# Performance work log

Measured on AMD Instinct MI355X. Metric: run time of the kernel, lower is better.

The kernel has to match this reference:

```python
import jax, jax.numpy as jnp
import numpy as np

V, E, H, B, T, O = 50000, 300, 512, 32, 256, 10


def setup_inputs() -> dict:
    key = jax.random.key(0)
    ks = jax.random.split(key, 12)
    sc = 1.0 / np.sqrt(H)  # torch LSTM init scale
    rn = lambda k, shape, s: (jax.random.normal(k, shape, jnp.float32) * s)
    return {
        "tokens": jax.random.randint(ks[0], (B, T), 0, V),
        "embed_table": rn(ks[1], (V, E), 0.1),
        "W_ih_f": rn(ks[2], (4 * H, E), sc),
        "W_hh_f": rn(ks[3], (4 * H, H), sc),
        "b_ih_f": rn(ks[4], (4 * H,), sc),
        "b_hh_f": rn(ks[5], (4 * H,), sc),
        "W_ih_b": rn(ks[6], (4 * H, E), sc),
        "W_hh_b": rn(ks[7], (4 * H, H), sc),
        "b_ih_b": rn(ks[8], (4 * H,), sc),
        "b_hh_b": rn(ks[9], (4 * H,), sc),
        "W_out": rn(ks[10], (O, 2 * H), 1.0 / np.sqrt(2 * H)),
        "b_out": rn(ks[11], (O,), 0.01),
    }


def _lstm_dir(x_tbe, W_ih, W_hh, b_ih, b_hh, reverse):
    """One LSTM direction. x_tbe: [T,B,E]. Returns hidden seq [T,B,H]."""
    Hd = W_hh.shape[1]
    # precompute input contribution for all timesteps: [T,B,4H]
    xg = jnp.einsum('tbe,ge->tbg', x_tbe, W_ih) + b_ih + b_hh

    def step(carry, xt):
        h, c = carry
        gates = xt + h @ W_hh.T                    # [B,4H]
        i, f, g, o = jnp.split(gates, 4, axis=-1)  # torch gate order i,f,g,o
        c = jax.nn.sigmoid(f) * c + jax.nn.sigmoid(i) * jnp.tanh(g)
        h = jax.nn.sigmoid(o) * jnp.tanh(c)
        return (h, c), h

    h0 = jnp.zeros((x_tbe.shape[1], Hd), x_tbe.dtype)
    _, hs = jax.lax.scan(step, (h0, h0), xg, reverse=reverse)
    return hs


def reference(tokens, embed_table, W_ih_f, W_hh_f, b_ih_f, b_hh_f,
              W_ih_b, W_hh_b, b_ih_b, b_hh_b, W_out, b_out):
    x = embed_table[tokens]          # [B,T,E] embedding lookup (dropout_e=0 in eval)
    x = x.transpose(1, 0, 2)         # [T,B,E] time-major, as in the torch module
    hf = _lstm_dir(x, W_ih_f, W_hh_f, b_ih_f, b_hh_f, reverse=False)
    hb = _lstm_dir(x, W_ih_b, W_hh_b, b_ih_b, b_hh_b, reverse=True)
    rnn_out = jnp.concatenate([hf, hb], axis=-1)   # [T,B,2H]
    # relu then max-pool over the full time axis (kernel = seq_len)
    pooled = jnp.max(jax.nn.relu(rnn_out), axis=0)  # [B,2H]
    logits = pooled @ W_out.T + b_out               # [B,O]
    return logits, rnn_out
```

## Files before the change

### kernel.cpp

```cpp
#include <hip/hip_runtime.h>
#include <hip/hip_bf16.h>

#define B_ 32
#define T_ 256
#define E_ 300
#define EP_ 320
#define H_ 512
#define O_ 10
#define TEAM 32
#define THR 512
#define HPB 16
#define NBLK 512

typedef __attribute__((ext_vector_type(8))) short bf16x8;
typedef __attribute__((ext_vector_type(4))) float f32x4;

__device__ __forceinline__ float bf2f(unsigned short u) {
  unsigned v = ((unsigned)u) << 16; float f; __builtin_memcpy(&f, &v, 4); return f;
}
__device__ __forceinline__ short f2bf(float x) {
  unsigned u; __builtin_memcpy(&u, &x, 4);
  unsigned r = u + 0x7fffu + ((u >> 16) & 1u);
  return (short)(r >> 16);
}

__global__ __launch_bounds__(256) void xprep_k(
    const int* __restrict__ tokens, const float* __restrict__ embed,
    unsigned short* __restrict__ xb)
{
  const int t = blockIdx.x;
  __shared__ int tok_s[B_];
  const int tid = threadIdx.x;
  if (tid < B_) tok_s[tid] = tokens[tid * T_ + t];
  __syncthreads();
  const size_t plane = (size_t)T_ * B_ * EP_;
  unsigned short* hi = xb;
  unsigned short* lo = xb + plane;
  for (int i = tid; i < B_ * E_; i += 256) {
    const int b = i / E_, e = i - b * E_;
    const float v = embed[(size_t)tok_s[b] * E_ + e];
    const short h = f2bf(v);
    const short l = f2bf(v - bf2f((unsigned short)h));
    const size_t o = ((size_t)t * B_ + b) * EP_ + e;
    hi[o] = (unsigned short)h; lo[o] = (unsigned short)l;
  }
  for (int i = tid; i < B_ * (EP_ - E_); i += 256) {
    const int b = i / (EP_ - E_), e = E_ + (i - b * (EP_ - E_));
    const size_t o = ((size_t)t * B_ + b) * EP_ + e;
    hi[o] = 0; lo[o] = 0;
  }
}

__global__ __launch_bounds__(320) void wprep_k(
    const float* __restrict__ Wf, const float* __restrict__ Wb,
    unsigned short* __restrict__ wp)
{
  const int row = blockIdx.x;
  const int dir = blockIdx.y;
  const int e   = threadIdx.x;
  const float* __restrict__ W = dir ? Wb : Wf;
  short h = 0, l = 0;
  if (e < E_) {
    const float v = W[(size_t)row * E_ + e];
    h = f2bf(v);
    l = f2bf(v - bf2f((unsigned short)h));
  }
  const size_t hiB = ((size_t)(dir * 2 + 0)) * 2048 * EP_;
  const size_t loB = ((size_t)(dir * 2 + 1)) * 2048 * EP_;
  wp[hiB + (size_t)row * EP_ + e] = (unsigned short)h;
  wp[loB + (size_t)row * EP_ + e] = (unsigned short)l;
}

__global__ __launch_bounds__(256) void xg_mfma_k(
    const unsigned short* __restrict__ wp,
    const unsigned short* __restrict__ xb,
    const float* __restrict__ bif, const float* __restrict__ bhf,
    const float* __restrict__ bib, const float* __restrict__ bhb,
    __hip_bfloat16* __restrict__ xg)
{
  const int rt  = blockIdx.x;
  const int t   = blockIdx.y;
  const int dir = blockIdx.z;
  const int tid = threadIdx.x;
  const int l = tid & 63, w = tid >> 6;
  const int m = l & 15, q = l >> 4;
  const int rowb = rt * 64 + w * 16;

  const float* __restrict__ bi = dir ? bib : bif;
  const float* __restrict__ bh = dir ? bhb : bhf;

  bf16x8 ahi[10], alo[10];
  {
    const unsigned short* whi =
        wp + ((size_t)(dir * 2 + 0) * 2048 + rowb + m) * EP_ + q * 8;
    const unsigned short* wlo =
        wp + ((size_t)(dir * 2 + 1) * 2048 + rowb + m) * EP_ + q * 8;
    #pragma unroll
    for (int kt = 0; kt < 10; ++kt) {
      ahi[kt] = *(const bf16x8*)(whi + kt * 32);
      alo[kt] = *(const bf16x8*)(wlo + kt * 32);
    }
  }

  const size_t plane = (size_t)T_ * B_ * EP_;
  const unsigned short* xh0 = xb + ((size_t)t * B_ + m     ) * EP_ + q * 8;
  const unsigned short* xh1 = xb + ((size_t)t * B_ + m + 16) * EP_ + q * 8;

  f32x4 acc0 = {0.f, 0.f, 0.f, 0.f}, acc1 = {0.f, 0.f, 0.f, 0.f};
  #pragma unroll
  for (int kt = 0; kt < 10; ++kt) {
    bf16x8 b0h = *(const bf16x8*)(xh0 + kt * 32);
    bf16x8 b0l = *(const bf16x8*)(xh0 + plane + kt * 32);
    bf16x8 b1h = *(const bf16x8*)(xh1 + kt * 32);
    bf16x8 b1l = *(const bf16x8*)(xh1 + plane + kt * 32);
    acc0 = __builtin_amdgcn_mfma_f32_16x16x32_bf16(ahi[kt], b0h, acc0, 0, 0, 0);
    acc0 = __builtin_amdgcn_mfma_f32_16x16x32_bf16(alo[kt], b0h, acc0, 0, 0, 0);
    acc0 = __builtin_amdgcn_mfma_f32_16x16x32_bf16(ahi[kt], b0l, acc0, 0, 0, 0);
    acc1 = __builtin_amdgcn_mfma_f32_16x16x32_bf16(ahi[kt], b1h, acc1, 0, 0, 0);
    acc1 = __builtin_amdgcn_mfma_f32_16x16x32_bf16(alo[kt], b1h, acc1, 0, 0, 0);
    acc1 = __builtin_amdgcn_mfma_f32_16x16x32_bf16(ahi[kt], b1l, acc1, 0, 0, 0);
  }

  const int r4 = rowb + q * 4;
  const float4 bi4 = *(const float4*)(bi + r4);
  const float4 bh4 = *(const float4*)(bh + r4);
  const float bias0 = bi4.x + bh4.x, bias1 = bi4.y + bh4.y;
  const float bias2 = bi4.z + bh4.z, bias3 = bi4.w + bh4.w;
  unsigned short* og =
      (unsigned short*)xg + ((size_t)(dir * T_ + t) * 2048 + r4) * B_;
  og[0 * B_ + m]      = (unsigned short)f2bf(acc0[0] + bias0);
  og[1 * B_ + m]      = (unsigned short)f2bf(acc0[1] + bias1);
  og[2 * B_ + m]      = (unsigned short)f2bf(acc0[2] + bias2);
  og[3 * B_ + m]      = (unsigned short)f2bf(acc0[3] + bias3);
  og[0 * B_ + m + 16] = (unsigned short)f2bf(acc1[0] + bias0);
  og[1 * B_ + m + 16] = (unsigned short)f2bf(acc1[1] + bias1);
  og[2 * B_ + m + 16] = (unsigned short)f2bf(acc1[2] + bias2);
  og[3 * B_ + m + 16] = (unsigned short)f2bf(acc1[3] + bias3);
}

__device__ __forceinline__ float sigm(float x)    { return 1.f / (1.f + __expf(-x)); }
__device__ __forceinline__ float tanhfast(float x){ return 1.f - 2.f / (__expf(2.f * x) + 1.f); }

__global__ __launch_bounds__(THR) void lstm_rec_k(
    const __hip_bfloat16* __restrict__ xg,
    const float* __restrict__ Whf, const float* __restrict__ Whb,
    unsigned short* __restrict__ ht,
    float* __restrict__ pooled,
    unsigned int* __restrict__ slots, unsigned int* __restrict__ elect)
{
  unsigned xcd;
  asm volatile("s_getreg_b32 %0, hwreg(HW_REG_XCC_ID)" : "=s"(xcd));
  xcd &= 7u;

  __shared__ unsigned rank_s;
  if (threadIdx.x == 0)
    rank_s = __hip_atomic_fetch_add(&elect[xcd], 1u, __ATOMIC_RELAXED,
                                    __HIP_MEMORY_SCOPE_AGENT);
  __syncthreads();
  const unsigned rank = rank_s;
  if (xcd > 1u || rank >= TEAM) return;
  const int dir = (int)xcd;

  const float* __restrict__ Wh = dir ? Whb : Whf;
  const int hs  = (int)rank * HPB;
  const int tid = threadIdx.x;
  const int l   = tid & 63;
  const int wid = tid >> 6;
  const int g   = wid & 3;
  const int kh  = wid >> 2;
  const int hh  = tid & 15, bb = tid >> 4;

  extern __shared__ char lds[];
  float* gp = (float*)(lds + 65536);

  bf16x8 ahi[8], alo[8];
  {
    const int m = l & 15, q = l >> 4;
    const float* wrow = Wh + (size_t)(g * H_ + hs + m) * H_ + kh * 256 + q * 8;
    #pragma unroll
    for (int kt = 0; kt < 8; ++kt) {
      const float* wp = wrow + kt * 32;
      #pragma unroll
      for (int j = 0; j < 8; ++j) {
        const float w = wp[j];
        const short hi = f2bf(w);
        ahi[kt][j] = hi;
        alo[kt][j] = f2bf(w - bf2f((unsigned short)hi));
      }
    }
  }

  const unsigned short* __restrict__ xgu = (const unsigned short*)xg;
  const size_t xco = ((size_t)hs + hh) * B_ + bb;

  float c_st = 0.f, pm = 0.f;

  for (int s = 0; s < T_; ++s) {
    const int tt = dir ? (T_ - 1 - s) : s;
    const size_t xb = (size_t)(dir * T_ + tt) * 2048 * B_;
    float x0 = bf2f(__builtin_nontemporal_load(xgu + xb + 0 * H_ * B_ + xco));
    float x1 = bf2f(__builtin_nontemporal_load(xgu + xb + 1 * H_ * B_ + xco));
    float x2 = bf2f(__builtin_nontemporal_load(xgu + xb + 2 * H_ * B_ + xco));
    float x3 = bf2f(__builtin_nontemporal_load(xgu + xb + 3 * H_ * B_ + xco));

    if (s > 0) {
      if (tid < 64) {
        unsigned v = 1u;
        const unsigned int* sp =
            slots + ((size_t)dir * T_ + (s - 1)) * TEAM + (tid & 31);
        int it = 0;
        do {
          if (tid < 32) {
            if (it < 16) {
              asm volatile("global_load_dword %0, %1, off sc0 nt\n\ts_waitcnt vmcnt(0)"
                           : "=v"(v) : "v"(sp) : "memory");
            } else {
              v = __hip_atomic_load(sp, __ATOMIC_RELAXED, __HIP_MEMORY_SCOPE_AGENT);
            }
          }
          ++it;
        } while (__ballot(v == 0u) != 0ull && it < (1 << 22));
      }
      __syncthreads();
      {
        const float4* src = (const float4*)(ht + (size_t)(dir * T_ + (s - 1)) * 32768);
        float4* dst = (float4*)lds;
        #pragma unroll
        for (int i = 0; i < 8; ++i)
          dst[tid + i * THR] = src[tid + i * THR];
      }
      __syncthreads();
      f32x4 acc0 = {0.f, 0.f, 0.f, 0.f}, acc1 = {0.f, 0.f, 0.f, 0.f};
      {
        const int n0 = l & 15;
        const int swz = (n0 & 7) << 4;
        const int kb = kh * 512 + (l >> 4) * 16;
        #pragma unroll
        for (int kt = 0; kt < 8; ++kt) {
          const int ko = kb + kt * 64;
          const char* p0 = lds + (((n0      ) * 1024 + ko) ^ swz);
          const char* p1 = lds + (((n0 + 16 ) * 1024 + ko) ^ swz);
          bf16x8 b0h = *(const bf16x8*)(p0);
          bf16x8 b0l = *(const bf16x8*)(p0 + 32768);
          bf16x8 b1h = *(const bf16x8*)(p1);
          bf16x8 b1l = *(const bf16x8*)(p1 + 32768);
          acc0 = __builtin_amdgcn_mfma_f32_16x16x32_bf16(ahi[kt], b0h, acc0, 0, 0, 0);
          acc0 = __builtin_amdgcn_mfma_f32_16x16x32_bf16(alo[kt], b0h, acc0, 0, 0, 0);
          acc0 = __builtin_amdgcn_mfma_f32_16x16x32_bf16(ahi[kt], b0l, acc0, 0, 0, 0);
          acc1 = __builtin_amdgcn_mfma_f32_16x16x32_bf16(ahi[kt], b1h, acc1, 0, 0, 0);
          acc1 = __builtin_amdgcn_mfma_f32_16x16x32_bf16(alo[kt], b1h, acc1, 0, 0, 0);
          acc1 = __builtin_amdgcn_mfma_f32_16x16x32_bf16(ahi[kt], b1l, acc1, 0, 0, 0);
        }
      }
      {
        const int slot = (kh * 4 + g) * 32;
        const int rowb = (l >> 4) * 4;
        #pragma unroll
        for (int r = 0; r < 4; ++r) {
          gp[(slot + (l & 15)     ) * 17 + rowb + r] = acc0[r];
          gp[(slot + 16 + (l & 15)) * 17 + rowb + r] = acc1[r];
        }
      }
      __syncthreads();
    }

    float Gi = x0, Gf = x1, Gg = x2, Go = x3;
    if (s > 0) {
      Gi += gp[(0 * 32 + bb) * 17 + hh] + gp[(4 * 32 + bb) * 17 + hh];
      Gf += gp[(1 * 32 + bb) * 17 + hh] + gp[(5 * 32 + bb) * 17 + hh];
      Gg += gp[(2 * 32 + bb) * 17 + hh] + gp[(6 * 32 + bb) * 17 + hh];
      Go += gp[(3 * 32 + bb) * 17 + hh] + gp[(7 * 32 + bb) * 17 + hh];
    }
    c_st = sigm(Gf) * c_st + sigm(Gi) * tanhfast(Gg);
    const float h = sigm(Go) * tanhfast(c_st);
    pm = fmaxf(pm, h);
    {
      const short hi = f2bf(h);
      const short lo = f2bf(h - bf2f((unsigned short)hi));
      char* base = (char*)(ht + (size_t)(dir * T_ + s) * 32768);
      const unsigned off = (unsigned)((bb * 1024 + (hs + hh) * 2) ^ ((bb & 7) << 4));
      *(unsigned short*)(base + off)         = (unsigned short)hi;
      *(unsigned short*)(base + 32768 + off) = (unsigned short)lo;
    }
    asm volatile("s_waitcnt vmcnt(0)" ::: "memory");
    __syncthreads();
    if (tid == 0) {
      unsigned int* mp = slots + ((size_t)dir * T_ + s) * TEAM + rank;
      unsigned one = 1u;
      asm volatile("global_store_dword %0, %1, off\n\ts_waitcnt vmcnt(0)"
                   :: "v"(mp), "v"(one) : "memory");
    }
  }
  pooled[(size_t)bb * 1024 + dir * H_ + hs + hh] = pm;
}

__global__ __launch_bounds__(256) void finalize_k(
    const unsigned short* __restrict__ ht, float* __restrict__ rnn)
{
  const int t = blockIdx.x, dir = blockIdx.y;
  const int s = dir ? (T_ - 1 - t) : t;
  const char* base = (const char*)(ht + (size_t)(dir * T_ + s) * 32768);
  const int b = threadIdx.x >> 3, c = threadIdx.x & 7;
  float* __restrict__ dst = rnn + ((size_t)t * B_ + b) * 1024 + dir * H_;
  #pragma unroll
  for (int j = 0; j < 8; ++j) {
    const int k0 = (c * 8 + j) * 8;
    const unsigned off = (unsigned)((b * 1024 + k0 * 2) ^ ((b & 7) << 4));
    bf16x8 hi = *(const bf16x8*)(base + off);
    bf16x8 lo = *(const bf16x8*)(base + 32768 + off);
    float4 o0, o1;
    o0.x = bf2f((unsigned short)hi[0]) + bf2f((unsigned short)lo[0]);
    o0.y = bf2f((unsigned short)hi[1]) + bf2f((unsigned short)lo[1]);
    o0.z = bf2f((unsigned short)hi[2]) + bf2f((unsigned short)lo[2]);
    o0.w = bf2f((unsigned short)hi[3]) + bf2f((unsigned short)lo[3]);
    o1.x = bf2f((unsigned short)hi[4]) + bf2f((unsigned short)lo[4]);
    o1.y = bf2f((unsigned short)hi[5]) + bf2f((unsigned short)lo[5]);
    o1.z = bf2f((unsigned short)hi[6]) + bf2f((unsigned short)lo[6]);
    o1.w = bf2f((unsigned short)hi[7]) + bf2f((unsigned short)lo[7]);
    *(float4*)(dst + k0)     = o0;
    *(float4*)(dst + k0 + 4) = o1;
  }
}

__global__ __launch_bounds__(64) void logits_k(
    const float* __restrict__ pooled, const float* __restrict__ Wout,
    const float* __restrict__ bout, float* __restrict__ out)
{
  const int b = blockIdx.x, lane = threadIdx.x;
  float acc[O_];
  #pragma unroll
  for (int o = 0; o < O_; ++o) acc[o] = 0.f;
  for (int k = lane; k < 2 * H_; k += 64) {
    const float pv = pooled[(size_t)b * 1024 + k];
    #pragma unroll
    for (int o = 0; o < O_; ++o) acc[o] += pv * Wout[(size_t)o * 1024 + k];
  }
  #pragma unroll
  for (int o = 0; o < O_; ++o) {
    float v = acc[o];
    #pragma unroll
    for (int off = 32; off > 0; off >>= 1) v += __shfl_down(v, off);
    if (lane == 0) out[b * O_ + o] = v + bout[o];
  }
}

extern "C" void kernel_launch(void* const* d_in, const int* in_sizes, int n_in,
                              void* d_out, int out_size, void* d_ws, size_t ws_size,
                              hipStream_t stream)
{
  const int*   tokens = (const int*)d_in[0];
  const float* embed  = (const float*)d_in[1];
  const float* Wihf   = (const float*)d_in[2];
  const float* Whhf   = (const float*)d_in[3];
  const float* bihf   = (const float*)d_in[4];
  const float* bhhf   = (const float*)d_in[5];
  const float* Wihb   = (const float*)d_in[6];
  const float* Whhb   = (const float*)d_in[7];
  const float* bihb   = (const float*)d_in[8];
  const float* bhhb   = (const float*)d_in[9];
  const float* Wout   = (const float*)d_in[10];
  const float* bout   = (const float*)d_in[11];
  float* out = (float*)d_out;

  char* ws = (char*)d_ws;
  const size_t XG_BYTES = (size_t)2 * T_ * 2048 * B_ * 2;
  const size_t HT_BYTES = (size_t)2 * T_ * 2 * B_ * H_ * 2;
  const size_t PL_BYTES = (size_t)B_ * 1024 * 4;
  const size_t SL_BYTES = (size_t)2 * T_ * TEAM * 4;
  const size_t EL_BYTES = 8 * 4;
  if (ws_size < XG_BYTES + HT_BYTES + PL_BYTES + SL_BYTES + EL_BYTES) return;

  __hip_bfloat16* xg     = (__hip_bfloat16*)ws;
  unsigned short* ht     = (unsigned short*)(ws + XG_BYTES);
  float*          pooled = (float*)(ws + XG_BYTES + HT_BYTES);
  unsigned int*   slots  = (unsigned int*)(ws + XG_BYTES + HT_BYTES + PL_BYTES);
  unsigned int*   elect  = (unsigned int*)(ws + XG_BYTES + HT_BYTES + PL_BYTES + SL_BYTES);

  unsigned short* xb = (unsigned short*)(ws + XG_BYTES);
  unsigned short* wpre = (unsigned short*)(ws + XG_BYTES + (size_t)2 * T_ * B_ * EP_ * 2);

  (void)hipMemsetAsync(slots, 0, SL_BYTES + EL_BYTES, stream);

  xprep_k<<<dim3(T_), 256, 0, stream>>>(tokens, embed, xb);
  wprep_k<<<dim3(2048, 2), 320, 0, stream>>>(Wihf, Wihb, wpre);
  xg_mfma_k<<<dim3(32, T_, 2), 256, 0, stream>>>(wpre, xb, bihf, bhhf, bihb, bhhb, xg);

  const int rec_lds = 82944;
  (void)hipFuncSetAttribute((const void*)lstm_rec_k,
                            hipFuncAttributeMaxDynamicSharedMemorySize, rec_lds);
  lstm_rec_k<<<dim3(NBLK), THR, rec_lds, stream>>>(xg, Whhf, Whhb, ht, pooled,
                                                   slots, elect);

  finalize_k<<<dim3(T_, 2), 256, 0, stream>>>(ht, out + B_ * O_);
  logits_k<<<dim3(B_), 64, 0, stream>>>(pooled, Wout, bout, out);
}
```

Before: 3.322 ms.

## Store per-block hidden-state slabs contiguously and swizzle during LDS load

```diff
diff --git a/kernel.cpp b/kernel.cpp
--- a/kernel.cpp
+++ b/kernel.cpp
@@ -224,10 +224,20 @@
       __syncthreads();
       {
         const float4* src = (const float4*)(ht + (size_t)(dir * T_ + (s - 1)) * 32768);
-        float4* dst = (float4*)lds;
         #pragma unroll
-        for (int i = 0; i < 8; ++i)
-          dst[tid + i * THR] = src[tid + i * THR];
+        for (int ii = 0; ii < 8; ++ii) {
+          const int i = tid + ii * THR;
+          const float4 v4 = src[i];
+          const int rk = i >> 7;
+          const int f  = i & 127;
+          const int pl = f >> 6;
+          const int j  = f & 63;
+          const int b  = j >> 1;
+          const int h0 = (j & 1) * 8;
+          const int dst = pl * 32768 +
+              ((b * 1024 + (rk * HPB + h0) * 2) ^ ((b & 7) << 4));
+          *(float4*)(lds + dst) = v4;
+        }
       }
       __syncthreads();
       f32x4 acc0 = {0.f, 0.f, 0.f, 0.f}, acc1 = {0.f, 0.f, 0.f, 0.f};
@@ -277,10 +287,10 @@
     {
       const short hi = f2bf(h);
       const short lo = f2bf(h - bf2f((unsigned short)hi));
-      char* base = (char*)(ht + (size_t)(dir * T_ + s) * 32768);
-      const unsigned off = (unsigned)((bb * 1024 + (hs + hh) * 2) ^ ((bb & 7) << 4));
-      *(unsigned short*)(base + off)         = (unsigned short)hi;
-      *(unsigned short*)(base + 32768 + off) = (unsigned short)lo;
+      unsigned short* region =
+          ht + (size_t)(dir * T_ + s) * 32768 + (size_t)rank * 1024;
+      region[tid]       = (unsigned short)hi;
+      region[512 + tid] = (unsigned short)lo;
     }
     asm volatile("s_waitcnt vmcnt(0)" ::: "memory");
     __syncthreads();
@@ -299,26 +309,20 @@
 {
   const int t = blockIdx.x, dir = blockIdx.y;
   const int s = dir ? (T_ - 1 - t) : t;
-  const char* base = (const char*)(ht + (size_t)(dir * T_ + s) * 32768);
+  const unsigned short* slab = ht + (size_t)(dir * T_ + s) * 32768;
   const int b = threadIdx.x >> 3, c = threadIdx.x & 7;
   float* __restrict__ dst = rnn + ((size_t)t * B_ + b) * 1024 + dir * H_;
   #pragma unroll
-  for (int j = 0; j < 8; ++j) {
-    const int k0 = (c * 8 + j) * 8;
-    const unsigned off = (unsigned)((b * 1024 + k0 * 2) ^ ((b & 7) << 4));
-    bf16x8 hi = *(const bf16x8*)(base + off);
-    bf16x8 lo = *(const bf16x8*)(base + 32768 + off);
-    float4 o0, o1;
-    o0.x = bf2f((unsigned short)hi[0]) + bf2f((unsigned short)lo[0]);
-    o0.y = bf2f((unsigned short)hi[1]) + bf2f((unsigned short)lo[1]);
-    o0.z = bf2f((unsigned short)hi[2]) + bf2f((unsigned short)lo[2]);
-    o0.w = bf2f((unsigned short)hi[3]) + bf2f((unsigned short)lo[3]);
-    o1.x = bf2f((unsigned short)hi[4]) + bf2f((unsigned short)lo[4]);
-    o1.y = bf2f((unsigned short)hi[5]) + bf2f((unsigned short)lo[5]);
-    o1.z = bf2f((unsigned short)hi[6]) + bf2f((unsigned short)lo[6]);
-    o1.w = bf2f((unsigned short)hi[7]) + bf2f((unsigned short)lo[7]);
-    *(float4*)(dst + k0)     = o0;
-    *(float4*)(dst + k0 + 4) = o1;
+  for (int j = 0; j < 16; ++j) {
+    const int k0 = c * 64 + j * 4;
+    const int rk = k0 >> 4;
+    const unsigned short* rg = slab + rk * 1024 + b * HPB + (k0 & 15);
+    float4 o;
+    o.x = bf2f(rg[0]) + bf2f(rg[512 + 0]);
+    o.y = bf2f(rg[1]) + bf2f(rg[512 + 1]);
+    o.z = bf2f(rg[2]) + bf2f(rg[512 + 2]);
+    o.w = bf2f(rg[3]) + bf2f(rg[512 + 3]);
+    *(float4*)(dst + k0) = o;
   }
 }
 
@@ -364,7 +368,7 @@
 
   char* ws = (char*)d_ws;
   const size_t XG_BYTES = (size_t)2 * T_ * 2048 * B_ * 2;
-  const size_t HT_BYTES = (size_t)2 * T_ * 2 * B_ * H_ * 2;
+  const size_t HT_BYTES = (size_t)2 * T_ * 32768 * 2;
   const size_t PL_BYTES = (size_t)B_ * 1024 * 4;
   const size_t SL_BYTES = (size_t)2 * T_ * TEAM * 4;
   const size_t EL_BYTES = 8 * 4;
```

Measured after the change: 3.309 ms. No clear change (-0.4%).
